# Optimization experiments

Measured on AMD Instinct MI355X. Metric: run time of the kernel, lower is better.

The kernel has to match this reference:

```python
import jax, jax.numpy as jnp
import numpy as np

B, S, H, DH = 2, 2048, 16, 64
D = H * DH  # 1024
NEG = 1e11

def setup_inputs() -> dict:
    key = jax.random.key(0)
    ks = jax.random.split(key, 4)
    std = 0.02
    return {
        "x": jax.random.normal(ks[0], (B, S, D), dtype=jnp.float32),
        "Wq": jax.random.normal(ks[1], (D, D), dtype=jnp.float32) * std,
        "bq": jnp.zeros((D,), dtype=jnp.float32),
        "Wk": jax.random.normal(ks[2], (D, D), dtype=jnp.float32) * std,
        "bk": jnp.zeros((D,), dtype=jnp.float32),
        "Wv": jax.random.normal(ks[3], (D, D), dtype=jnp.float32) * std,
        "bv": jnp.zeros((D,), dtype=jnp.float32),
    }

def reference(x, Wq, bq, Wk, bk, Wv, bv):
    # QKV projections: [B,S,D]
    q = x @ Wq + bq
    k = x @ Wk + bk
    v = x @ Wv + bv
    # split heads -> [B,H,S,DH]
    def split(t):
        return t.reshape(B, S, H, DH).transpose(0, 2, 1, 3)
    q, k, v = split(q), split(k), split(v)
    # scaled scores [B,H,S,S]
    scores = jnp.einsum("bhqd,bhkd->bhqk", q, k) / jnp.sqrt(jnp.float32(DH))
    # causal mask: query i attends to keys j <= i; original does s*m - (1-m)*1e11
    m = (jnp.arange(S)[:, None] >= jnp.arange(S)[None, :]).astype(scores.dtype)
    scores = scores * m - (1.0 - m) * NEG
    probs = jax.nn.softmax(scores, axis=-1)
    out = jnp.einsum("bhqk,bhkd->bhqd", probs, v)  # [B,H,S,DH]
    return out.transpose(0, 2, 1, 3).reshape(B, S, D)
```

## Files before the change

kernel.cpp:

```cpp
#include <hip/hip_runtime.h>
#include <hip/hip_bf16.h>
#include <stdint.h>

#define B_    2
#define S_    2048
#define H_    16
#define DH_   64
#define D_    1024
#define ND3   3072
#define MTOT  4096
#define L2E   1.4426950408889634f
#define MASKVAL (-3.0e38f)
#define SBIAS   (-14.0f)

typedef __attribute__((ext_vector_type(8))) short bf16x8;
typedef __attribute__((ext_vector_type(4))) short bf16x4;
typedef __attribute__((ext_vector_type(4))) float f32x4;

__device__ inline short f2bs(float f) {
  __hip_bfloat16 h = __float2bfloat16(f);
  return *reinterpret_cast<short*>(&h);
}

__device__ inline void gl_lds16(const void* g, void* l) {
  __builtin_amdgcn_global_load_lds(
      (const __attribute__((address_space(1))) uint32_t*)g,
      (__attribute__((address_space(3))) uint32_t*)l, 16, 0, 0);
}

__global__ __launch_bounds__(256) void prep_kernel(
    const float* __restrict__ X, const float* __restrict__ Wq,
    const float* __restrict__ Wk, const float* __restrict__ Wv,
    short* __restrict__ Xb, short* __restrict__ Wt) {
  __shared__ float t[32][33];
  int bid = blockIdx.x;
  if (bid < 4096) {
    const int i = (bid * 256 + threadIdx.x) * 4;
    float4 v = *reinterpret_cast<const float4*>(X + i);
    bf16x4 o;
    o[0] = f2bs(v.x); o[1] = f2bs(v.y); o[2] = f2bs(v.z); o[3] = f2bs(v.w);
    *reinterpret_cast<bf16x4*>(Xb + i) = o;
  } else {
    bid -= 4096;
    const int z = bid >> 10;
    const int rem = bid & 1023;
    const int n0 = (rem & 31) * 32, k0 = (rem >> 5) * 32;
    const int x = threadIdx.x & 31, y = threadIdx.x >> 5;
    const float* W = z == 0 ? Wq : (z == 1 ? Wk : Wv);
    short* out = Wt + (size_t)z * (D_ * D_);
#pragma unroll
    for (int i = 0; i < 4; ++i)
      t[y + 8 * i][x] = W[(size_t)(k0 + y + 8 * i) * D_ + n0 + x];
    __syncthreads();
#pragma unroll
    for (int i = 0; i < 4; ++i)
      out[(size_t)(n0 + y + 8 * i) * D_ + k0 + x] = f2bs(t[x][y + 8 * i]);
  }
}

__global__ __launch_bounds__(512, 2) void qkv_gemm_kernel(
    const short* __restrict__ Xb, const short* __restrict__ Wt,
    const float* __restrict__ bq, const float* __restrict__ bk,
    const float* __restrict__ bv, short* __restrict__ QKV,
    short* __restrict__ Vt) {
  __shared__ char Lds[114688];
  const int tid = threadIdx.x;
  const int lane = tid & 63;
  const int wid = tid >> 6;
  const int l15 = lane & 15, lg = lane >> 4;
  const int wm = wid >> 2, wn = wid & 3;
  const int bid = blockIdx.x;
  const int wgid = (bid & 7) * 32 + (bid >> 3);
  const int m0 = (wgid >> 4) * 256, n0 = (wgid & 15) * 192;

  const int srow = tid >> 3;
  const int scol = ((tid & 7) ^ (srow & 7)) * 8;
  const short* pa = Xb + (size_t)(m0 + srow) * D_ + scol;
  const short* pb = Wt + (size_t)(n0 + srow) * D_ + scol;
  char* sdst = Lds + (tid & 448) * 16;

  const int abase = wm * 16384;
  int a_off[8][2], b_off[3][2];
#pragma unroll
  for (int mr = 0; mr < 8; ++mr)
#pragma unroll
    for (int ks = 0; ks < 2; ++ks)
      a_off[mr][ks] =
          (mr * 16 + l15) * 128 + ((((ks * 4 + lg)) ^ (l15 & 7)) << 4);
#pragma unroll
  for (int nr = 0; nr < 3; ++nr)
#pragma unroll
    for (int ks = 0; ks < 2; ++ks)
      b_off[nr][ks] = (wn * 48 + nr * 16 + l15) * 128 +
                      ((((ks * 4 + lg)) ^ (l15 & 7)) << 4);

  f32x4 acc[8][3];
#pragma unroll
  for (int i = 0; i < 8; ++i)
#pragma unroll
    for (int j = 0; j < 3; ++j) acc[i][j] = (f32x4){0.f, 0.f, 0.f, 0.f};

#define BARRIER()                                                             \
  __builtin_amdgcn_s_barrier();                                               \
  __builtin_amdgcn_sched_barrier(0)

  gl_lds16(pa, sdst);
  gl_lds16(pa + (size_t)64 * D_, sdst + 8192);
  gl_lds16(pa + (size_t)128 * D_, sdst + 16384);
  gl_lds16(pa + (size_t)192 * D_, sdst + 24576);
  gl_lds16(pb, sdst + 32768);
  gl_lds16(pb + (size_t)64 * D_, sdst + 40960);
  gl_lds16(pb + (size_t)128 * D_, sdst + 49152);
  asm volatile("s_waitcnt vmcnt(0)" ::: "memory");
  BARRIER();

#define TILE(J, DL)                                                           \
  {                                                                           \
    const int j_ = (J);                                                       \
    const bool stg = (j_ + 1 < 16);                                           \
    const int RD = (DL) * 57344;                                              \
    const int WD = (1 - (DL)) * 57344;                                        \
    const short* pa1 = pa + (j_ + 1) * 64;                                    \
    const short* pb1 = pb + (j_ + 1) * 64;                                    \
    bf16x8 af[4], bf0, bf1, bf2;                                              \
       \
    if (stg) {                                                                \
      gl_lds16(pa1, sdst + WD);                                               \
      gl_lds16(pa1 + (size_t)64 * D_, sdst + WD + 8192);                      \
    }                                                                         \
    bf0 = *reinterpret_cast<const bf16x8*>(Lds + RD + 32768 + b_off[0][0]);   \
    bf1 = *reinterpret_cast<const bf16x8*>(Lds + RD + 32768 + b_off[1][0]);   \
    bf2 = *reinterpret_cast<const bf16x8*>(Lds + RD + 32768 + b_off[2][0]);   \
    _Pragma("unroll") for (int mr = 0; mr < 4; ++mr) af[mr] =                 \
        *reinterpret_cast<const bf16x8*>(Lds + RD + abase + a_off[mr][0]);    \
    BARRIER();                                                                \
    __builtin_amdgcn_s_setprio(1);                                            \
    _Pragma("unroll") for (int mr = 0; mr < 4; ++mr) {                        \
      acc[mr][0] = __builtin_amdgcn_mfma_f32_16x16x32_bf16(af[mr], bf0,       \
                                                           acc[mr][0], 0, 0,  \
                                                           0);                \
      acc[mr][1] = __builtin_amdgcn_mfma_f32_16x16x32_bf16(af[mr], bf1,       \
                                                           acc[mr][1], 0, 0,  \
                                                           0);                \
      acc[mr][2] = __builtin_amdgcn_mfma_f32_16x16x32_bf16(af[mr], bf2,       \
                                                           acc[mr][2], 0, 0,  \
                                                           0);                \
    }                                                                         \
    __builtin_amdgcn_s_setprio(0);                                            \
    BARRIER();                                                                \
             \
    if (stg) {                                                                \
      gl_lds16(pa1 + (size_t)128 * D_, sdst + WD + 16384);                    \
      gl_lds16(pa1 + (size_t)192 * D_, sdst + WD + 24576);                    \
    }                                                                         \
    _Pragma("unroll") for (int mr = 0; mr < 4; ++mr) af[mr] =                 \
        *reinterpret_cast<const bf16x8*>(Lds + RD + abase +                   \
                                         a_off[mr + 4][0]);                   \
    BARRIER();                                                                \
    __builtin_amdgcn_s_setprio(1);                                            \
    _Pragma("unroll") for (int mr = 0; mr < 4; ++mr) {                        \
      acc[mr + 4][0] = __builtin_amdgcn_mfma_f32_16x16x32_bf16(               \
          af[mr], bf0, acc[mr + 4][0], 0, 0, 0);                              \
      acc[mr + 4][1] = __builtin_amdgcn_mfma_f32_16x16x32_bf16(               \
          af[mr], bf1, acc[mr + 4][1], 0, 0, 0);                              \
      acc[mr + 4][2] = __builtin_amdgcn_mfma_f32_16x16x32_bf16(               \
          af[mr], bf2, acc[mr + 4][2], 0, 0, 0);                              \
    }                                                                         \
    __builtin_amdgcn_s_setprio(0);                                            \
    BARRIER();                                                                \
       \
    if (stg) {                                                                \
      gl_lds16(pb1, sdst + WD + 32768);                                       \
      gl_lds16(pb1 + (size_t)64 * D_, sdst + WD + 40960);                     \
      gl_lds16(pb1 + (size_t)128 * D_, sdst + WD + 49152);                    \
    }                                                                         \
    bf0 = *reinterpret_cast<const bf16x8*>(Lds + RD + 32768 + b_off[0][1]);   \
    bf1 = *reinterpret_cast<const bf16x8*>(Lds + RD + 32768 + b_off[1][1]);   \
    bf2 = *reinterpret_cast<const bf16x8*>(Lds + RD + 32768 + b_off[2][1]);   \
    _Pragma("unroll") for (int mr = 0; mr < 4; ++mr) af[mr] =                 \
        *reinterpret_cast<const bf16x8*>(Lds + RD + abase + a_off[mr][1]);    \
    BARRIER();                                                                \
    __builtin_amdgcn_s_setprio(1);                                            \
    _Pragma("unroll") for (int mr = 0; mr < 4; ++mr) {                        \
      acc[mr][0] = __builtin_amdgcn_mfma_f32_16x16x32_bf16(af[mr], bf0,       \
                                                           acc[mr][0], 0, 0,  \
                                                           0);                \
      acc[mr][1] = __builtin_amdgcn_mfma_f32_16x16x32_bf16(af[mr], bf1,       \
                                                           acc[mr][1], 0, 0,  \
                                                           0);                \
      acc[mr][2] = __builtin_amdgcn_mfma_f32_16x16x32_bf16(af[mr], bf2,       \
                                                           acc[mr][2], 0, 0,  \
                                                           0);                \
    }                                                                         \
    __builtin_amdgcn_s_setprio(0);                                            \
    BARRIER();                                                                \
               \
    _Pragma("unroll") for (int mr = 0; mr < 4; ++mr) af[mr] =                 \
        *reinterpret_cast<const bf16x8*>(Lds + RD + abase +                   \
                                         a_off[mr + 4][1]);                   \
    BARRIER();                                                                \
    __builtin_amdgcn_s_setprio(1);                                            \
    _Pragma("unroll") for (int mr = 0; mr < 4; ++mr) {                        \
      acc[mr + 4][0] = __builtin_amdgcn_mfma_f32_16x16x32_bf16(               \
          af[mr], bf0, acc[mr + 4][0], 0, 0, 0);                              \
      acc[mr + 4][1] = __builtin_amdgcn_mfma_f32_16x16x32_bf16(               \
          af[mr], bf1, acc[mr + 4][1], 0, 0, 0);                              \
      acc[mr + 4][2] = __builtin_amdgcn_mfma_f32_16x16x32_bf16(               \
          af[mr], bf2, acc[mr + 4][2], 0, 0, 0);                              \
    }                                                                         \
    __builtin_amdgcn_s_setprio(0);                                            \
    asm volatile("s_waitcnt vmcnt(0)" ::: "memory");                          \
    BARRIER();                                                                \
  }

  for (int jj = 0; jj < 16; jj += 2) {
    TILE(jj, 0);
    TILE(jj + 1, 1);
  }
#undef TILE
#undef BARRIER

  const int wr = wm * 128;
#pragma unroll
  for (int nr = 0; nr < 3; ++nr) {
    const int col = n0 + wn * 48 + nr * 16 + l15;
    if (col < 2 * D_) {
      float bias, qs;
      if (col < D_) { bias = bq[col];      qs = 0.125f * L2E; }
      else          { bias = bk[col - D_]; qs = 1.f; }
#pragma unroll
      for (int mr = 0; mr < 8; ++mr)
#pragma unroll
        for (int r = 0; r < 4; ++r) {
          const int row = m0 + wr + mr * 16 + lg * 4 + r;
          QKV[(size_t)row * ND3 + col] = f2bs((acc[mr][nr][r] + bias) * qs);
        }
    } else {
      const int f = col - 2 * D_;
      const float bias = bv[f];
      const int bb = m0 >> 11;
      const int srow_base = (m0 & 2047) + wr + lg * 4;
      short* vout = Vt + ((size_t)(bb * H_ + (f >> 6)) * DH_ + (f & 63)) * S_;
#pragma unroll
      for (int mr = 0; mr < 8; ++mr) {
        bf16x4 pv;
#pragma unroll
        for (int r = 0; r < 4; ++r) pv[r] = f2bs(acc[mr][nr][r] + bias);
        *reinterpret_cast<bf16x4*>(vout + srow_base + mr * 16) = pv;
      }
    }
  }
}

__global__ __launch_bounds__(256, 4) void attn_kernel(
    const short* __restrict__ QKV, const short* __restrict__ Vtg,
    float* __restrict__ Out) {
  __shared__ short KV[5][4096];
  const int tid = threadIdx.x;
  const int lane = tid & 63, wid = tid >> 6;
  const int l15 = lane & 15, lg = lane >> 4;
  const int bh = blockIdx.x;
  const int qt = (S_ / 64 - 1) - (int)blockIdx.y;
  const int b = bh >> 4, h = bh & 15;
  const int q0 = qt * 64;
  const short* Qg = QKV + (size_t)b * S_ * ND3 + h * DH_;
  const short* Kg = QKV + (size_t)b * S_ * ND3 + D_ + h * DH_;
  const short* Vg = Vtg + (size_t)bh * DH_ * S_;

  const int srow = tid >> 3;
  const int scol = ((tid & 7) ^ (srow & 7)) * 8;
  const char* kbase = (const char*)&KV[0][0];
  char* dst = (char*)kbase + (tid & 192) * 16;
  int ka[2];
#pragma unroll
  for (int ks = 0; ks < 2; ++ks)
    ka[ks] = l15 * 128 + ((((ks * 4 + lg)) ^ (l15 & 7)) << 4);
  int va[4];
#pragma unroll
  for (int ntk = 0; ntk < 4; ++ntk)
    va[ntk] = l15 * 128 + (((2 * ntk + (lg >> 1)) ^ (l15 & 7)) << 4) +
              ((lg & 1) << 3);
  const int qrow_g = q0 + wid * 16 + l15;

  bf16x8 qf[2];
#pragma unroll
  for (int ks = 0; ks < 2; ++ks)
    qf[ks] = *reinterpret_cast<const bf16x8*>(Qg + (size_t)qrow_g * ND3 +
                                              ks * 32 + lg * 8);

  f32x4 o[4];
#pragma unroll
  for (int i = 0; i < 4; ++i) o[i] = (f32x4){0.f, 0.f, 0.f, 0.f};
  float lsum = 0.f;

  const short* kp = Kg + (size_t)srow * ND3 + scol;
  const short* vp = Vg + (size_t)srow * S_ + scol;

#define STAGE_AT(KOFF, VOFF)                                                  \
  {                                                                           \
    gl_lds16(kp, dst + (KOFF));                                               \
    gl_lds16(kp + 32 * ND3, dst + (KOFF) + 4096);                             \
    gl_lds16(vp, dst + (VOFF));                                               \
    gl_lds16(vp + 32 * S_, dst + (VOFF) + 4096);                              \
    kp += 64 * ND3;                                                           \
    vp += 64;                                                                 \
  }

  int kr = 8192, kw = 0;
  int vr = 16384, vw = 32768;

  STAGE_AT(0, 16384);
  if (qt >= 1) STAGE_AT(8192, 24576);
  asm volatile("s_waitcnt vmcnt(0)" ::: "memory");
  __builtin_amdgcn_s_barrier();
  __builtin_amdgcn_sched_barrier(0);

  f32x4 sA[4], sB[4];
#pragma unroll
  for (int i = 0; i < 4; ++i) sA[i] = (f32x4){SBIAS, SBIAS, SBIAS, SBIAS};
#pragma unroll
  for (int ks = 0; ks < 2; ++ks)
#pragma unroll
    for (int nt = 0; nt < 4; ++nt) {
      const bf16x8 kf =
          *reinterpret_cast<const bf16x8*>(kbase + ka[ks] + nt * 2048);
      sA[nt] = __builtin_amdgcn_mfma_f32_16x16x32_bf16(kf, qf[ks], sA[nt],
                                                       0, 0, 0);
    }

#define STEP_BODY(T, SC, SN)                                                  \
  {                                                                           \
    const int T_ = (T);                                                       \
    if (T_ + 2 <= qt) STAGE_AT(kw, vw);                                       \
    if (T_ + 1 <= qt) {                                                       \
      _Pragma("unroll") for (int i = 0; i < 4; ++i)                           \
          SN[i] = (f32x4){SBIAS, SBIAS, SBIAS, SBIAS};                        \
      _Pragma("unroll") for (int ks = 0; ks < 2; ++ks)                        \
        _Pragma("unroll") for (int nt = 0; nt < 4; ++nt) {                    \
          const bf16x8 kf = *reinterpret_cast<const bf16x8*>(                 \
              kbase + kr + ka[ks] + nt * 2048);                               \
          SN[nt] = __builtin_amdgcn_mfma_f32_16x16x32_bf16(kf, qf[ks],        \
                                                           SN[nt], 0, 0, 0);  \
        }                                                                     \
    }                                                                         \
    if (T_ == qt) {                         \
      const int kv0 = T_ * 64;                                                \
      _Pragma("unroll") for (int nt = 0; nt < 4; ++nt)                        \
        _Pragma("unroll") for (int r = 0; r < 4; ++r)                         \
          if (kv0 + nt * 16 + lg * 4 + r > qrow_g) SC[nt][r] = MASKVAL;       \
    }                                                                         \
    float rowsum = 0.f;                                                       \
    bf16x4 pk[4];                                                             \
    _Pragma("unroll") for (int nt = 0; nt < 4; ++nt) {                        \
      const float p0 = exp2f(SC[nt][0]);                                      \
      const float p1 = exp2f(SC[nt][1]);                                      \
      const float p2 = exp2f(SC[nt][2]);                                      \
      const float p3 = exp2f(SC[nt][3]);                                      \
      rowsum += (p0 + p1) + (p2 + p3);                                        \
      union { uint32_t u[2]; bf16x4 v; } pu;                                  \
      pu.u[0] = (__float_as_uint(p1) & 0xffff0000u) |                         \
                (__float_as_uint(p0) >> 16);                                  \
      pu.u[1] = (__float_as_uint(p3) & 0xffff0000u) |                         \
                (__float_as_uint(p2) >> 16);                                  \
      pk[nt] = pu.v;                                                          \
    }                                                                         \
    lsum += rowsum;                                                           \
    _Pragma("unroll") for (int ntk = 0; ntk < 4; ++ntk)                       \
      _Pragma("unroll") for (int ntd = 0; ntd < 4; ++ntd) {                   \
        const bf16x4 vf = *reinterpret_cast<const bf16x4*>(                   \
            kbase + vr + va[ntk] + ntd * 2048);                               \
        o[ntd] = __builtin_amdgcn_mfma_f32_16x16x16bf16_1k(vf, pk[ntk],       \
                                                           o[ntd], 0, 0, 0);  \
      }                                                                       \
    if (T_ < qt) {                                                            \
      asm volatile("s_waitcnt vmcnt(0)" ::: "memory");                        \
      __builtin_amdgcn_s_barrier();                                           \
      __builtin_amdgcn_sched_barrier(0);                                      \
    }                                                                         \
    kr ^= 8192; kw ^= 8192;                                                   \
    { const int tv = vr; vr = 73728 - vr - vw; vw = tv; }                     \
  }

  for (int t = 0; t <= qt; t += 2) {
    STEP_BODY(t, sA, sB);
    if (t + 1 <= qt) STEP_BODY(t + 1, sB, sA);
  }
#undef STEP_BODY
#undef STAGE_AT

  float ls = lsum;
  ls += __shfl_xor(ls, 16);
  ls += __shfl_xor(ls, 32);
  const float inv = 1.f / ls;
#pragma unroll
  for (int nt = 0; nt < 4; ++nt) {
    f32x4 v = {o[nt][0] * inv, o[nt][1] * inv, o[nt][2] * inv, o[nt][3] * inv};
    *reinterpret_cast<f32x4*>(
        &Out[((size_t)b * S_ + qrow_g) * D_ + h * DH_ + nt * 16 + lg * 4]) = v;
  }
}

extern "C" void kernel_launch(void* const* d_in, const int* in_sizes, int n_in,
                              void* d_out, int out_size, void* d_ws,
                              size_t ws_size, hipStream_t stream) {
  const float* x  = (const float*)d_in[0];
  const float* Wq = (const float*)d_in[1];
  const float* bq = (const float*)d_in[2];
  const float* Wk = (const float*)d_in[3];
  const float* bk = (const float*)d_in[4];
  const float* Wv = (const float*)d_in[5];
  const float* bv = (const float*)d_in[6];
  float* out = (float*)d_out;

  char* ws = (char*)d_ws;
  short* xb  = (short*)(ws);
  short* Wt  = (short*)(ws + 8388608);
  short* qkv = (short*)(ws + 14680064);
  short* Vt  = (short*)(ws + 39845888);

  prep_kernel<<<dim3(4096 + 3072), dim3(256), 0, stream>>>(x, Wq, Wk, Wv, xb,
                                                           Wt);
  qkv_gemm_kernel<<<dim3(256), dim3(512), 0, stream>>>(xb, Wt, bq, bk, bv,
                                                       qkv, Vt);
  attn_kernel<<<dim3(B_ * H_, S_ / 64), dim3(256), 0, stream>>>(qkv, Vt, out);
}
```

Baseline: 79.42 us.

## Permute V^T store layout for 16-byte LDS reads and rebalance GEMM prefetch

The QKV projection now writes V^T with sequence positions permuted within each 64-block, so the attention kernel can read two PV MFMA operands with one 16-byte LDS load instead of two 8-byte loads. The addressing reuses the K swizzle offsets and drops the separate V offset table. The GEMM main loop also moves the B-tile global-to-LDS prefetch earlier, splitting it across the first two phases to even out in-flight loads. The risk is that the permutation must match exactly between producer and consumer, and the earlier issue raises outstanding memory traffic during the first compute phases.

```diff
diff --git a/kernel.cpp b/kernel.cpp
--- a/kernel.cpp
+++ b/kernel.cpp
@@ -127,6 +127,8 @@
     if (stg) {                                                                \
       gl_lds16(pa1, sdst + WD);                                               \
       gl_lds16(pa1 + (size_t)64 * D_, sdst + WD + 8192);                      \
+      gl_lds16(pb1, sdst + WD + 32768);                                       \
+      gl_lds16(pb1 + (size_t)64 * D_, sdst + WD + 40960);                     \
     }                                                                         \
     bf0 = *reinterpret_cast<const bf16x8*>(Lds + RD + 32768 + b_off[0][0]);   \
     bf1 = *reinterpret_cast<const bf16x8*>(Lds + RD + 32768 + b_off[1][0]);   \
@@ -148,10 +150,11 @@
     }                                                                         \
     __builtin_amdgcn_s_setprio(0);                                            \
     BARRIER();                                                                \
-             \
+                  \
     if (stg) {                                                                \
       gl_lds16(pa1 + (size_t)128 * D_, sdst + WD + 16384);                    \
       gl_lds16(pa1 + (size_t)192 * D_, sdst + WD + 24576);                    \
+      gl_lds16(pb1 + (size_t)128 * D_, sdst + WD + 49152);                    \
     }                                                                         \
     _Pragma("unroll") for (int mr = 0; mr < 4; ++mr) af[mr] =                 \
         *reinterpret_cast<const bf16x8*>(Lds + RD + abase +                   \
@@ -168,12 +171,7 @@
     }                                                                         \
     __builtin_amdgcn_s_setprio(0);                                            \
     BARRIER();                                                                \
-       \
-    if (stg) {                                                                \
-      gl_lds16(pb1, sdst + WD + 32768);                                       \
-      gl_lds16(pb1 + (size_t)64 * D_, sdst + WD + 40960);                     \
-      gl_lds16(pb1 + (size_t)128 * D_, sdst + WD + 49152);                    \
-    }                                                                         \
+                           \
     bf0 = *reinterpret_cast<const bf16x8*>(Lds + RD + 32768 + b_off[0][1]);   \
     bf1 = *reinterpret_cast<const bf16x8*>(Lds + RD + 32768 + b_off[1][1]);   \
     bf2 = *reinterpret_cast<const bf16x8*>(Lds + RD + 32768 + b_off[2][1]);   \
@@ -238,15 +236,18 @@
     } else {
       const int f = col - 2 * D_;
       const float bias = bv[f];
-      const int bb = m0 >> 11;
-      const int srow_base = (m0 & 2047) + wr + lg * 4;
-      short* vout = Vt + ((size_t)(bb * H_ + (f >> 6)) * DH_ + (f & 63)) * S_;
+      const int base0 = (m0 & 2047) + wr;
+      short* vout = Vt + ((size_t)((m0 >> 11) * H_ + (f >> 6)) * DH_ +
+                          (f & 63)) * S_;
 #pragma unroll
       for (int mr = 0; mr < 8; ++mr) {
         bf16x4 pv;
 #pragma unroll
         for (int r = 0; r < 4; ++r) pv[r] = f2bs(acc[mr][nr][r] + bias);
-        *reinterpret_cast<bf16x4*>(vout + srow_base + mr * 16) = pv;
+        const int ntk = mr & 3;
+        const int s_new = base0 + (mr >> 2) * 64 +
+                          ((ntk >> 1) * 4 + lg) * 8 + (ntk & 1) * 4;
+        *reinterpret_cast<bf16x4*>(vout + s_new) = pv;
       }
     }
   }
@@ -275,11 +276,6 @@
 #pragma unroll
   for (int ks = 0; ks < 2; ++ks)
     ka[ks] = l15 * 128 + ((((ks * 4 + lg)) ^ (l15 & 7)) << 4);
-  int va[4];
-#pragma unroll
-  for (int ntk = 0; ntk < 4; ++ntk)
-    va[ntk] = l15 * 128 + (((2 * ntk + (lg >> 1)) ^ (l15 & 7)) << 4) +
-              ((lg & 1) << 3);
   const int qrow_g = q0 + wid * 16 + l15;
 
   bf16x8 qf[2];
@@ -365,12 +361,16 @@
       pk[nt] = pu.v;                                                          \
     }                                                                         \
     lsum += rowsum;                                                           \
-    _Pragma("unroll") for (int ntk = 0; ntk < 4; ++ntk)                       \
+    _Pragma("unroll") for (int p = 0; p < 2; ++p)                             \
       _Pragma("unroll") for (int ntd = 0; ntd < 4; ++ntd) {                   \
-        const bf16x4 vf = *reinterpret_cast<const bf16x4*>(                   \
-            kbase + vr + va[ntk] + ntd * 2048);                               \
-        o[ntd] = __builtin_amdgcn_mfma_f32_16x16x16bf16_1k(vf, pk[ntk],       \
+        const bf16x8 vf8 = *reinterpret_cast<const bf16x8*>(                  \
+            kbase + vr + ka[p] + ntd * 2048);                                 \
+        const bf16x4 vlo = __builtin_shufflevector(vf8, vf8, 0, 1, 2, 3);     \
+        const bf16x4 vhi = __builtin_shufflevector(vf8, vf8, 4, 5, 6, 7);     \
+        o[ntd] = __builtin_amdgcn_mfma_f32_16x16x16bf16_1k(vlo, pk[2 * p],    \
                                                            o[ntd], 0, 0, 0);  \
+        o[ntd] = __builtin_amdgcn_mfma_f32_16x16x16bf16_1k(                   \
+            vhi, pk[2 * p + 1], o[ntd], 0, 0, 0);                             \
       }                                                                       \
     if (T_ < qt) {                                                            \
       asm volatile("s_waitcnt vmcnt(0)" ::: "memory");                        \
```

Result: faster. 77.01 us (-3.0%).
